# Performance work log

Measured on AMD Instinct MI355X. Metric: run time of the kernel, lower is better.

## Reference

```python
import jax, jax.numpy as jnp
import numpy as np

B_SZ, N_NODES, C_IN, C_OUT, M_EDGES, DEG = 32, 4096, 64, 64, 64, 256
E_INC = M_EDGES * DEG  # 16384 incidences
NEG_SLOPE = 0.2
MARGIN = 4.2


def setup_inputs() -> dict:
    key = jax.random.key(0)
    k1, k2, k3, k4 = jax.random.split(key, 4)
    x = jax.random.normal(k1, (B_SZ, N_NODES, C_IN), jnp.float32)
    # glorot-ish params
    weight = jax.random.normal(k2, (C_IN, C_OUT), jnp.float32) * (1.0 / np.sqrt(C_IN))
    att = jax.random.normal(k3, (1, 1, 2 * C_OUT), jnp.float32) * 0.1
    node_ids = jax.random.randint(k4, (E_INC,), 0, N_NODES, dtype=jnp.int32)
    edge_ids = jnp.repeat(jnp.arange(M_EDGES, dtype=jnp.int32), DEG)  # sorted, all edges present
    hyperedge_index = jnp.stack([node_ids, edge_ids], axis=0)
    return {"x": x, "weight": weight, "att": att,
            "hyperedge_index": hyperedge_index,
            "num_edges": M_EDGES, "num_nodes": N_NODES}


def _segment_softmax(scores, seg, num_segments):
    m = jax.ops.segment_max(scores, seg, num_segments=num_segments)
    e = jnp.exp(scores - m[seg])
    s = jax.ops.segment_sum(e, seg, num_segments=num_segments)
    return e / s[seg]


def reference(x, weight, att, hyperedge_index, num_edges, num_nodes):
    node_ids = hyperedge_index[0]
    edge_ids = hyperedge_index[1]
    M = num_edges
    N = num_nodes

    xw = jnp.einsum('bnc,cd->bnd', x, weight)       # [B,N,C]
    x1 = jnp.swapaxes(xw, 0, 1)                     # [N,B,C]

    x_i = x1[node_ids]                              # [E,B,C] gather per incidence
    edge_sums = jax.ops.segment_sum(x_i, edge_ids, num_segments=M,
                                    indices_are_sorted=True)  # [M,B,C]
    x_j = edge_sums[edge_ids]                       # [E,B,C]

    # pairwise hyperedge contrastive loss (vectorized double loop over edges)
    inner = jnp.einsum('kbc,mbc->kmb', edge_sums, edge_sums)          # [M,M,B]
    nrm = jnp.linalg.norm(edge_sums, axis=-1)                         # [M,B]
    cos = inner / (nrm[:, None, :] * nrm[None, :, :])                 # [M,M,B]
    diff = edge_sums[:, None] - edge_sums[None, :]                    # [M,M,B,C]
    dist = jnp.linalg.norm(diff, axis=-1)                             # [M,M,B]
    loss_item = cos * dist + (1.0 - cos) * jnp.clip(MARGIN - dist, 0.0)
    loss_hyper = jnp.sum(jnp.abs(jnp.mean(loss_item, axis=2))) / (M + 1) ** 2

    # GAT-style attention over incidences, softmax grouped by node
    cat = jnp.concatenate([x_i, x_j], axis=-1)                        # [E,B,2C]
    scores = jnp.sum(cat * att[0], axis=-1)                           # [E,B] (heads=1)
    scores = jax.nn.leaky_relu(scores, negative_slope=NEG_SLOPE)
    alpha = _segment_softmax(scores, node_ids, N)                     # [E,B]
    # dropout omitted (eval mode)

    ones = jnp.ones((node_ids.shape[0],), xw.dtype)
    D = jax.ops.segment_sum(ones, node_ids, num_segments=N)           # node degree
    deg_e = jax.ops.segment_sum(ones, edge_ids, num_segments=M, indices_are_sorted=True)
    B_norm = jnp.where(deg_e > 0, 1.0 / deg_e, 0.0)                   # 1/edge degree, inf->0

    # stage 1: nodes -> hyperedges (source_to_target)
    msg1 = B_norm[edge_ids][:, None, None] * (alpha[..., None] * x_i) # [E,B,C]
    out_e = jax.ops.segment_sum(msg1, edge_ids, num_segments=M, indices_are_sorted=True)
    # stage 2: hyperedges -> nodes (target_to_source)
    msg2 = D[node_ids][:, None, None] * (alpha[..., None] * out_e[edge_ids])
    out_n = jax.ops.segment_sum(msg2, node_ids, num_segments=N)       # [N,B,C]

    out = jnp.swapaxes(out_n, 0, 1)                                   # [B,N,C]
    constrain_total = jnp.abs(jnp.mean(x_i - x_j)) + loss_hyper
    return out, constrain_total
```

## Files before the change

kernel.cpp:

```cpp
#include <hip/hip_runtime.h>
#include <hip/hip_fp16.h>
#include <math.h>

#define B_SZ 32
#define N_NODES 4096
#define C_DIM 64
#define M_EDGES 64
#define DEG 256
#define E_INC 16384
#define NEG_SLOPE 0.2f
#define MARGIN 4.2f

__device__ __forceinline__ float wsum64(float v) {
#pragma unroll
  for (int off = 32; off > 0; off >>= 1) v += __shfl_xor(v, off, 64);
  return v;
}

__global__ __launch_bounds__(256) void k_p0(
    const float* __restrict__ x, const float* __restrict__ w,
    const float* __restrict__ att, const int* __restrict__ node_ids,
    float* __restrict__ s1_t, __half* __restrict__ xh,
    int* __restrict__ cntv) {
  const int bid = blockIdx.x;
  const int t = threadIdx.x;
  if (bid < 1024) {
    __shared__ float part[4][64];
    __shared__ float wattl[64];
    const int kk = t & 63, q = t >> 6;
    float p = 0.f;
#pragma unroll
    for (int c = 0; c < 16; ++c)
      p = fmaf(w[kk * 64 + q * 16 + c], att[q * 16 + c], p);
    part[q][kk] = p;
    __syncthreads();
    if (t < 64)
      wattl[t] = part[0][t] + part[1][t] + part[2][t] + part[3][t];
    __syncthreads();
    const int lane = t & 63, wv = t >> 6;
    const int kq = lane & 15, rsub = lane >> 4;
    const float4 wq = ((const float4*)wattl)[kq];
    const int r0 = bid * 128 + wv * 32;
#pragma unroll 4
    for (int it = 0; it < 8; ++it) {
      const int row = r0 + it * 4 + rsub;
      const float4 xv = ((const float4*)x)[row * 16 + kq];
      float vv = xv.x * wq.x + xv.y * wq.y + xv.z * wq.z + xv.w * wq.w;
      vv += __shfl_xor(vv, 1, 64);
      vv += __shfl_xor(vv, 2, 64);
      vv += __shfl_xor(vv, 4, 64);
      vv += __shfl_xor(vv, 8, 64);
      if (kq == 0) {
        const int n = row & (N_NODES - 1);
        const int b = row >> 12;
        s1_t[n * 32 + b] = vv;
      }
      union {
        __half2 h2[2];
        uint2 u;
      } pk;
      pk.h2[0] = __halves2half2(__float2half(xv.x), __float2half(xv.y));
      pk.h2[1] = __halves2half2(__float2half(xv.z), __float2half(xv.w));
      ((uint2*)xh)[row * 16 + kq] = pk.u;
    }
  } else {
    __shared__ int cnt[N_NODES];
    const int m = bid - 1024;
#pragma unroll
    for (int i = 0; i < 16; ++i) cnt[t + 256 * i] = 0;
    __syncthreads();
    atomicAdd(&cnt[node_ids[m * DEG + t]], 1);
    __syncthreads();
#pragma unroll
    for (int i = 0; i < 16; ++i)
      cntv[m * N_NODES + t + 256 * i] = cnt[t + 256 * i];
  }
}

__global__ __launch_bounds__(256) void k_p1(
    const __half* __restrict__ xh, const float* __restrict__ w,
    const float* __restrict__ att, const int* __restrict__ node_ids,
    float* __restrict__ es_t, float* __restrict__ s2,
    float* __restrict__ nrm2, float* __restrict__ essum) {
  __shared__ float wl[4096];
  __shared__ float sx[4][64];
  __shared__ float part2[4][64];
  const int bid = blockIdx.x;
  const int t = threadIdx.x;
  const int b = 4 * (bid & 7) + ((bid >> 3) & 3);
  const int m = bid >> 5;
  const int lane = t & 63, wv = t >> 6;
  const int co = lane & 7, rg = lane >> 3;
  float4* wl4 = (float4*)wl;
  const float4* w4 = (const float4*)w;
#pragma unroll
  for (int i = 0; i < 4; ++i) wl4[t + 256 * i] = w4[t + 256 * i];
  const uint4* xb = (const uint4*)(xh + (size_t)b * (N_NODES * C_DIM));
  const int myinc = node_ids[m * DEG + wv * 64 + lane];
  int nds[8];
#pragma unroll
  for (int j = 0; j < 8; ++j) nds[j] = __shfl(myinc, j * 8 + rg, 64);
  uint4 v[8];
#pragma unroll
  for (int j = 0; j < 8; ++j) v[j] = xb[nds[j] * 8 + co];
  float acc[8] = {0.f, 0.f, 0.f, 0.f, 0.f, 0.f, 0.f, 0.f};
#pragma unroll
  for (int j = 0; j < 8; ++j) {
    const __half2* hp = (const __half2*)&v[j];
#pragma unroll
    for (int q = 0; q < 4; ++q) {
      const float2 f2 = __half22float2(hp[q]);
      acc[2 * q] += f2.x;
      acc[2 * q + 1] += f2.y;
    }
  }
#pragma unroll
  for (int off = 8; off < 64; off <<= 1) {
#pragma unroll
    for (int k = 0; k < 8; ++k) acc[k] += __shfl_xor(acc[k], off, 64);
  }
  if (rg == 0) {
    ((float4*)&sx[wv][co * 8])[0] =
        make_float4(acc[0], acc[1], acc[2], acc[3]);
    ((float4*)&sx[wv][co * 8])[1] =
        make_float4(acc[4], acc[5], acc[6], acc[7]);
  }
  __syncthreads();
  {
    const int c = t & 63;
    float ep = 0.f;
#pragma unroll
    for (int jj = 0; jj < 16; ++jj) {
      const int j = wv * 16 + jj;
      const float sxcj = sx[0][j] + sx[1][j] + sx[2][j] + sx[3][j];
      ep = fmaf(sxcj, wl[j * 64 + c], ep);
    }
    part2[wv][c] = ep;
  }
  __syncthreads();
  if (t < 64) {
    const float es = part2[0][t] + part2[1][t] + part2[2][t] + part2[3][t];
    es_t[(m * 64 + t) * 32 + b] = es;
    const float sr = wsum64(es * att[64 + t]);
    const float nr = wsum64(es * es);
    const float er = wsum64(es);
    if (t == 0) {
      s2[m * 32 + b] = sr;
      nrm2[m * 32 + b] = nr;
      essum[m * 32 + b] = er;
    }
  }
}

__global__ __launch_bounds__(256) void k_p2(
    const float* __restrict__ es_t, const float* __restrict__ nrm2,
    const int* __restrict__ cntv, const float* __restrict__ s1_t,
    const float* __restrict__ s2, float* __restrict__ lossbuf2,
    float2* __restrict__ pnb, int* __restrict__ pdat,
    int* __restrict__ plen) {
  const int bid = blockIdx.x;
  if (bid < 504) {
    const int wv = threadIdx.x >> 6;
    const int p = bid * 4 + wv;
    int k = 0, off = 0;
    while (off + (63 - k) <= p) {
      off += 63 - k;
      ++k;
    }
    const int m = k + 1 + (p - off);
    const int lane = threadIdx.x & 63;
    const int b = lane & 31, ch = lane >> 5;
    float inner = 0.f;
#pragma unroll 8
    for (int cc = 0; cc < 32; ++cc) {
      const int c = cc + 32 * ch;
      inner = fmaf(es_t[(k * 64 + c) * 32 + b], es_t[(m * 64 + c) * 32 + b],
                   inner);
    }
    inner += __shfl_xor(inner, 32, 64);
    const float nk2 = nrm2[k * 32 + b];
    const float nm2 = nrm2[m * 32 + b];
    const float d2 = fmaxf(nk2 + nm2 - 2.f * inner, 0.f);
    const float dist = sqrtf(d2);
    const float cosv = inner / sqrtf(nk2 * nm2);
    float li = cosv * dist + (1.f - cosv) * fmaxf(MARGIN - dist, 0.f);
#pragma unroll
    for (int o = 16; o > 0; o >>= 1) li += __shfl_xor(li, o, 64);
    if (lane == 0) lossbuf2[p] = 2.f * fabsf(li * (1.f / 32.f));
  } else {
    const int idx = (bid - 504) * 256 + threadIdx.x;
    const int n = idx >> 5, b = idx & 31;
    const float s1v = s1_t[n * 32 + b];
    const bool leader = (b == 0);
    float mx = -1e30f, S = 0.f;
    int j = 0, Dsum = 0;
#pragma unroll 4
    for (int m = 0; m < 64; ++m) {
      const int cm = cntv[m * N_NODES + n];
      float sc = s1v + s2[m * 32 + b];
      sc = sc > 0.f ? sc : NEG_SLOPE * sc;
      const float scv = (cm > 0) ? sc : -1e30f;
      const float nm = fmaxf(mx, scv);
      S = S * __expf(mx - nm) + (float)cm * __expf(scv - nm);
      mx = nm;
      if (leader) {
        if (cm > 0) {
          pdat[n * 64 + j] = m | (cm << 8);
          ++j;
        }
        Dsum += cm;
      }
    }
    if (leader) plen[n] = j | (Dsum << 7);
    float2 pv;
    pv.x = mx;
    pv.y = (S > 0.f) ? 1.f / S : 0.f;
    pnb[n * 32 + b] = pv;
  }
}

__global__ __launch_bounds__(256) void k_p3(
    const __half* __restrict__ xh, const int* __restrict__ node_ids,
    const float* __restrict__ w, const float* __restrict__ s1_t,
    const float* __restrict__ s2, const float2* __restrict__ pnb,
    const float* __restrict__ essum, const float* __restrict__ lossbuf2,
    float* __restrict__ out_e_t, float* __restrict__ outs) {
  __shared__ float wl[4096];
  __shared__ float sx[4][64];
  __shared__ float part2[4][64];
  const int bid = blockIdx.x;
  const int t = threadIdx.x;
  if (bid < 2048) {
    const int b = 4 * (bid & 7) + ((bid >> 3) & 3);
    const int m = bid >> 5;
    const int lane = t & 63, wv = t >> 6;
    const int co = lane & 7, rg = lane >> 3;
    float4* wl4 = (float4*)wl;
    const float4* w4 = (const float4*)w;
#pragma unroll
    for (int i = 0; i < 4; ++i) wl4[t + 256 * i] = w4[t + 256 * i];
    const uint4* xb = (const uint4*)(xh + (size_t)b * (N_NODES * C_DIM));
    const float s2mb = s2[m * 32 + b];
    const int myinc = node_ids[m * DEG + wv * 64 + lane];
    const float s1v = s1_t[myinc * 32 + b];
    const float2 pv = pnb[myinc * 32 + b];
    float scl = s1v + s2mb;
    scl = scl > 0.f ? scl : NEG_SLOPE * scl;
    const float mya = __expf(scl - pv.x) * pv.y;
    int nds[8];
    float av[8];
#pragma unroll
    for (int j = 0; j < 8; ++j) {
      nds[j] = __shfl(myinc, j * 8 + rg, 64);
      av[j] = __shfl(mya, j * 8 + rg, 64);
    }
    uint4 v[8];
#pragma unroll
    for (int j = 0; j < 8; ++j) v[j] = xb[nds[j] * 8 + co];
    float acc[8] = {0.f, 0.f, 0.f, 0.f, 0.f, 0.f, 0.f, 0.f};
#pragma unroll
    for (int j = 0; j < 8; ++j) {
      const __half2* hp = (const __half2*)&v[j];
#pragma unroll
      for (int q = 0; q < 4; ++q) {
        const float2 f2 = __half22float2(hp[q]);
        acc[2 * q] = fmaf(av[j], f2.x, acc[2 * q]);
        acc[2 * q + 1] = fmaf(av[j], f2.y, acc[2 * q + 1]);
      }
    }
#pragma unroll
    for (int off = 8; off < 64; off <<= 1) {
#pragma unroll
      for (int k = 0; k < 8; ++k) acc[k] += __shfl_xor(acc[k], off, 64);
    }
    if (rg == 0) {
      ((float4*)&sx[wv][co * 8])[0] =
          make_float4(acc[0], acc[1], acc[2], acc[3]);
      ((float4*)&sx[wv][co * 8])[1] =
          make_float4(acc[4], acc[5], acc[6], acc[7]);
    }
    __syncthreads();
    {
      const int c = t & 63;
      float ep = 0.f;
#pragma unroll
      for (int jj = 0; jj < 16; ++jj) {
        const int j = wv * 16 + jj;
        const float sxcj = sx[0][j] + sx[1][j] + sx[2][j] + sx[3][j];
        ep = fmaf(sxcj, wl[j * 64 + c], ep);
      }
      part2[wv][c] = ep;
    }
    __syncthreads();
    if (t < 64) {
      const float oc = part2[0][t] + part2[1][t] + part2[2][t] + part2[3][t];
      out_e_t[(m * 64 + t) * 32 + b] = oc * (1.0f / 256.0f);
    }
  } else {
    __shared__ float smf[256];
    float s = 0.f;
    for (int i = t; i < M_EDGES * B_SZ; i += 256) s += essum[i];
    smf[t] = s;
    __syncthreads();
    for (int o = 128; o > 0; o >>= 1) {
      if (t < o) smf[t] += smf[t + o];
      __syncthreads();
    }
    const float S = smf[0];
    __syncthreads();
    float l = 0.f;
    for (int i = t; i < 2016; i += 256) l += lossbuf2[i];
    smf[t] = l;
    __syncthreads();
    for (int o = 128; o > 0; o >>= 1) {
      if (t < o) smf[t] += smf[t + o];
      __syncthreads();
    }
    if (t == 0) {
      const float mean = S * (-255.0f) / 33554432.0f;
      outs[0] = fabsf(mean) + smf[0] * (1.0f / 4225.0f);
    }
  }
}

__global__ __launch_bounds__(256) void k_p4(
    const int* __restrict__ plen, const int* __restrict__ pdat,
    const float* __restrict__ s1_t, const float* __restrict__ s2,
    const float2* __restrict__ pnb, const float* __restrict__ out_e_t,
    float* __restrict__ out) {
  __shared__ int lme[64];
  __shared__ float lcnt[64];
  __shared__ float al[64][32];
  const int n = blockIdx.x;
  const int t = threadIdx.x;
  const int pl = plen[n];
  const int len = pl & 127;
  const float Dn = (float)(pl >> 7);
  const int c = t & 63, bq = t >> 6;
  const size_t nb = (size_t)n * 64 + c;
  const size_t st = (size_t)N_NODES * 64;
  if (len == 0) {
#pragma unroll
    for (int j = 0; j < 8; ++j) out[(bq * 8 + j) * st + nb] = 0.f;
    return;
  }
  if (t < len) {
    const int pe = pdat[n * 64 + t];
    lme[t] = pe & 63;
    lcnt[t] = (float)(pe >> 8);
  }
  __syncthreads();
  {
    const int b = t & 31, lq = t >> 5;
    const float s1v = s1_t[n * 32 + b];
    const float2 pv = pnb[n * 32 + b];
    for (int base = 0; base < len; base += 8) {
      const int li = base + lq;
      if (li < len) {
        const int m = lme[li];
        float sc = s1v + s2[m * 32 + b];
        sc = sc > 0.f ? sc : NEG_SLOPE * sc;
        al[li][b] = lcnt[li] * __expf(sc - pv.x) * pv.y;
      }
    }
  }
  __syncthreads();
  float4 a0 = {0.f, 0.f, 0.f, 0.f}, a1 = {0.f, 0.f, 0.f, 0.f};
  for (int li = 0; li < len; ++li) {
    const int m = lme[li];
    const float4 v0 = *(const float4*)&out_e_t[(m * 64 + c) * 32 + bq * 8];
    const float4 v1 = *(const float4*)&out_e_t[(m * 64 + c) * 32 + bq * 8 + 4];
    const float* alr = al[li];
    a0.x = fmaf(alr[bq * 8 + 0], v0.x, a0.x);
    a0.y = fmaf(alr[bq * 8 + 1], v0.y, a0.y);
    a0.z = fmaf(alr[bq * 8 + 2], v0.z, a0.z);
    a0.w = fmaf(alr[bq * 8 + 3], v0.w, a0.w);
    a1.x = fmaf(alr[bq * 8 + 4], v1.x, a1.x);
    a1.y = fmaf(alr[bq * 8 + 5], v1.y, a1.y);
    a1.z = fmaf(alr[bq * 8 + 6], v1.z, a1.z);
    a1.w = fmaf(alr[bq * 8 + 7], v1.w, a1.w);
  }
  out[(bq * 8 + 0) * st + nb] = Dn * a0.x;
  out[(bq * 8 + 1) * st + nb] = Dn * a0.y;
  out[(bq * 8 + 2) * st + nb] = Dn * a0.z;
  out[(bq * 8 + 3) * st + nb] = Dn * a0.w;
  out[(bq * 8 + 4) * st + nb] = Dn * a1.x;
  out[(bq * 8 + 5) * st + nb] = Dn * a1.y;
  out[(bq * 8 + 6) * st + nb] = Dn * a1.z;
  out[(bq * 8 + 7) * st + nb] = Dn * a1.w;
}

extern "C" void kernel_launch(void* const* d_in, const int* in_sizes, int n_in,
                              void* d_out, int out_size, void* d_ws,
                              size_t ws_size, hipStream_t stream) {
  (void)in_sizes; (void)n_in; (void)out_size; (void)ws_size;
  const float* x = (const float*)d_in[0];
  const float* weight = (const float*)d_in[1];
  const float* att = (const float*)d_in[2];
  const int* node_ids = (const int*)d_in[3];
  float* out = (float*)d_out;

  char* wsb = (char*)d_ws;
  float* es_t = (float*)(wsb);
  float* out_e_t = (float*)(wsb + (512 << 10));
  float* s1_t = (float*)(wsb + (1024 << 10));
  int* cntv = (int*)(wsb + (1536 << 10));
  float2* pnb = (float2*)(wsb + (2560 << 10));
  int* pdat = (int*)(wsb + (3584 << 10));
  float* s2 = (float*)(wsb + (4608 << 10));
  float* nrm2 = (float*)(wsb + (4616 << 10));
  float* essum = (float*)(wsb + (4624 << 10));
  float* lossbuf2 = (float*)(wsb + (4632 << 10));
  int* plen = (int*)(wsb + (4640 << 10));
  __half* xh = (__half*)(wsb + (5120 << 10));

  k_p0<<<1088, 256, 0, stream>>>(x, weight, att, node_ids, s1_t, xh, cntv);
  k_p1<<<2048, 256, 0, stream>>>(xh, weight, att, node_ids, es_t, s2, nrm2,
                                 essum);
  k_p2<<<1016, 256, 0, stream>>>(es_t, nrm2, cntv, s1_t, s2, lossbuf2, pnb,
                                 pdat, plen);
  k_p3<<<2049, 256, 0, stream>>>(xh, node_ids, weight, s1_t, s2, pnb, essum,
                                 lossbuf2, out_e_t,
                                 out + (size_t)B_SZ * N_NODES * C_DIM);
  k_p4<<<4096, 256, 0, stream>>>(plen, pdat, s1_t, s2, pnb, out_e_t, out);
}
```

Measured before the change: 88.32 us.

## Process four batches per block in edge-aggregation kernels and halve p0 grid

k_p1 and k_p3 now handle four batch indices per block instead of one. The shared-memory weight load, the node-id loads and the softmax-parameter loads are amortised across those batches, and the results go out as float4 stores into the batch-minor layout. The W projection is restructured so each wave computes a full 64-length dot product for one batch, instead of splitting the reduction across waves. k_p0 gives each block twice as many rows. Grids shrink fourfold for the edge kernels, which lowers parallelism and latency hiding.

```diff
diff --git a/kernel.cpp b/kernel.cpp
--- a/kernel.cpp
+++ b/kernel.cpp
@@ -24,7 +24,7 @@
     int* __restrict__ cntv) {
   const int bid = blockIdx.x;
   const int t = threadIdx.x;
-  if (bid < 1024) {
+  if (bid < 512) {
     __shared__ float part[4][64];
     __shared__ float wattl[64];
     const int kk = t & 63, q = t >> 6;
@@ -40,9 +40,9 @@
     const int lane = t & 63, wv = t >> 6;
     const int kq = lane & 15, rsub = lane >> 4;
     const float4 wq = ((const float4*)wattl)[kq];
-    const int r0 = bid * 128 + wv * 32;
+    const int r0 = bid * 256 + wv * 64;
 #pragma unroll 4
-    for (int it = 0; it < 8; ++it) {
+    for (int it = 0; it < 16; ++it) {
       const int row = r0 + it * 4 + rsub;
       const float4 xv = ((const float4*)x)[row * 16 + kq];
       float vv = xv.x * wq.x + xv.y * wq.y + xv.z * wq.z + xv.w * wq.w;
@@ -65,7 +65,7 @@
     }
   } else {
     __shared__ int cnt[N_NODES];
-    const int m = bid - 1024;
+    const int m = bid - 512;
 #pragma unroll
     for (int i = 0; i < 16; ++i) cnt[t + 256 * i] = 0;
     __syncthreads();
@@ -83,72 +83,77 @@
     float* __restrict__ es_t, float* __restrict__ s2,
     float* __restrict__ nrm2, float* __restrict__ essum) {
   __shared__ float wl[4096];
-  __shared__ float sx[4][64];
-  __shared__ float part2[4][64];
+  __shared__ float sx[4][4][64];
+  __shared__ float est[4][64];
   const int bid = blockIdx.x;
+  const int bg = bid & 7;
+  const int m = bid >> 3;
+  const int b0 = bg * 4;
   const int t = threadIdx.x;
-  const int b = 4 * (bid & 7) + ((bid >> 3) & 3);
-  const int m = bid >> 5;
   const int lane = t & 63, wv = t >> 6;
   const int co = lane & 7, rg = lane >> 3;
   float4* wl4 = (float4*)wl;
   const float4* w4 = (const float4*)w;
 #pragma unroll
   for (int i = 0; i < 4; ++i) wl4[t + 256 * i] = w4[t + 256 * i];
-  const uint4* xb = (const uint4*)(xh + (size_t)b * (N_NODES * C_DIM));
   const int myinc = node_ids[m * DEG + wv * 64 + lane];
   int nds[8];
 #pragma unroll
   for (int j = 0; j < 8; ++j) nds[j] = __shfl(myinc, j * 8 + rg, 64);
-  uint4 v[8];
-#pragma unroll
-  for (int j = 0; j < 8; ++j) v[j] = xb[nds[j] * 8 + co];
-  float acc[8] = {0.f, 0.f, 0.f, 0.f, 0.f, 0.f, 0.f, 0.f};
-#pragma unroll
-  for (int j = 0; j < 8; ++j) {
-    const __half2* hp = (const __half2*)&v[j];
-#pragma unroll
-    for (int q = 0; q < 4; ++q) {
-      const float2 f2 = __half22float2(hp[q]);
-      acc[2 * q] += f2.x;
-      acc[2 * q + 1] += f2.y;
-    }
-  }
-#pragma unroll
-  for (int off = 8; off < 64; off <<= 1) {
-#pragma unroll
-    for (int k = 0; k < 8; ++k) acc[k] += __shfl_xor(acc[k], off, 64);
-  }
-  if (rg == 0) {
-    ((float4*)&sx[wv][co * 8])[0] =
-        make_float4(acc[0], acc[1], acc[2], acc[3]);
-    ((float4*)&sx[wv][co * 8])[1] =
-        make_float4(acc[4], acc[5], acc[6], acc[7]);
+#pragma unroll
+  for (int bi = 0; bi < 4; ++bi) {
+    const uint4* xb =
+        (const uint4*)(xh + (size_t)(b0 + bi) * (N_NODES * C_DIM));
+    uint4 v[8];
+#pragma unroll
+    for (int j = 0; j < 8; ++j) v[j] = xb[nds[j] * 8 + co];
+    float acc[8] = {0.f, 0.f, 0.f, 0.f, 0.f, 0.f, 0.f, 0.f};
+#pragma unroll
+    for (int j = 0; j < 8; ++j) {
+      const __half2* hp = (const __half2*)&v[j];
+#pragma unroll
+      for (int q = 0; q < 4; ++q) {
+        const float2 f2 = __half22float2(hp[q]);
+        acc[2 * q] += f2.x;
+        acc[2 * q + 1] += f2.y;
+      }
+    }
+#pragma unroll
+    for (int off = 8; off < 64; off <<= 1) {
+#pragma unroll
+      for (int k = 0; k < 8; ++k) acc[k] += __shfl_xor(acc[k], off, 64);
+    }
+    if (rg == 0) {
+      ((float4*)&sx[wv][bi][co * 8])[0] =
+          make_float4(acc[0], acc[1], acc[2], acc[3]);
+      ((float4*)&sx[wv][bi][co * 8])[1] =
+          make_float4(acc[4], acc[5], acc[6], acc[7]);
+    }
   }
   __syncthreads();
   {
-    const int c = t & 63;
-    float ep = 0.f;
-#pragma unroll
-    for (int jj = 0; jj < 16; ++jj) {
-      const int j = wv * 16 + jj;
-      const float sxcj = sx[0][j] + sx[1][j] + sx[2][j] + sx[3][j];
-      ep = fmaf(sxcj, wl[j * 64 + c], ep);
-    }
-    part2[wv][c] = ep;
+    const int c = lane;
+    float es = 0.f;
+#pragma unroll 8
+    for (int j = 0; j < 64; ++j) {
+      const float sxcj =
+          sx[0][wv][j] + sx[1][wv][j] + sx[2][wv][j] + sx[3][wv][j];
+      es = fmaf(sxcj, wl[j * 64 + c], es);
+    }
+    est[wv][c] = es;
+    const float sr = wsum64(es * att[64 + c]);
+    const float nr = wsum64(es * es);
+    const float er = wsum64(es);
+    if (c == 0) {
+      s2[m * 32 + b0 + wv] = sr;
+      nrm2[m * 32 + b0 + wv] = nr;
+      essum[m * 32 + b0 + wv] = er;
+    }
   }
   __syncthreads();
   if (t < 64) {
-    const float es = part2[0][t] + part2[1][t] + part2[2][t] + part2[3][t];
-    es_t[(m * 64 + t) * 32 + b] = es;
-    const float sr = wsum64(es * att[64 + t]);
-    const float nr = wsum64(es * es);
-    const float er = wsum64(es);
-    if (t == 0) {
-      s2[m * 32 + b] = sr;
-      nrm2[m * 32 + b] = nr;
-      essum[m * 32 + b] = er;
-    }
+    const float4 o = make_float4(est[0][t], est[1][t], est[2][t], est[3][t]);
+    *(float4*)&es_t[(m * 64 + t) * 32 + b0] = o;
   }
 }
 
@@ -226,75 +231,90 @@
     const float* __restrict__ essum, const float* __restrict__ lossbuf2,
     float* __restrict__ out_e_t, float* __restrict__ outs) {
   __shared__ float wl[4096];
-  __shared__ float sx[4][64];
-  __shared__ float part2[4][64];
+  __shared__ float sx[4][4][64];
+  __shared__ float est[4][64];
   const int bid = blockIdx.x;
   const int t = threadIdx.x;
-  if (bid < 2048) {
-    const int b = 4 * (bid & 7) + ((bid >> 3) & 3);
-    const int m = bid >> 5;
+  if (bid < 512) {
+    const int bg = bid & 7;
+    const int m = bid >> 3;
+    const int b0 = bg * 4;
     const int lane = t & 63, wv = t >> 6;
     const int co = lane & 7, rg = lane >> 3;
     float4* wl4 = (float4*)wl;
     const float4* w4 = (const float4*)w;
 #pragma unroll
     for (int i = 0; i < 4; ++i) wl4[t + 256 * i] = w4[t + 256 * i];
-    const uint4* xb = (const uint4*)(xh + (size_t)b * (N_NODES * C_DIM));
-    const float s2mb = s2[m * 32 + b];
     const int myinc = node_ids[m * DEG + wv * 64 + lane];
-    const float s1v = s1_t[myinc * 32 + b];
-    const float2 pv = pnb[myinc * 32 + b];
-    float scl = s1v + s2mb;
-    scl = scl > 0.f ? scl : NEG_SLOPE * scl;
-    const float mya = __expf(scl - pv.x) * pv.y;
+    const float4 s14 = *(const float4*)&s1_t[myinc * 32 + b0];
+    const float* pp = (const float*)&pnb[myinc * 32 + b0];
+    const float4 pA = *(const float4*)pp;
+    const float4 pB = *(const float4*)(pp + 4);
+    float mya[4];
+    {
+      const float s1a[4] = {s14.x, s14.y, s14.z, s14.w};
+      const float mxa[4] = {pA.x, pA.z, pB.x, pB.z};
+      const float iva[4] = {pA.y, pA.w, pB.y, pB.w};
+#pragma unroll
+      for (int bi = 0; bi < 4; ++bi) {
+        float sc = s1a[bi] + s2[m * 32 + b0 + bi];
+        sc = sc > 0.f ? sc : NEG_SLOPE * sc;
+        mya[bi] = __expf(sc - mxa[bi]) * iva[bi];
+      }
+    }
     int nds[8];
-    float av[8];
-#pragma unroll
-    for (int j = 0; j < 8; ++j) {
-      nds[j] = __shfl(myinc, j * 8 + rg, 64);
-      av[j] = __shfl(mya, j * 8 + rg, 64);
-    }
-    uint4 v[8];
-#pragma unroll
-    for (int j = 0; j < 8; ++j) v[j] = xb[nds[j] * 8 + co];
-    float acc[8] = {0.f, 0.f, 0.f, 0.f, 0.f, 0.f, 0.f, 0.f};
-#pragma unroll
-    for (int j = 0; j < 8; ++j) {
-      const __half2* hp = (const __half2*)&v[j];
-#pragma unroll
-      for (int q = 0; q < 4; ++q) {
-        const float2 f2 = __half22float2(hp[q]);
-        acc[2 * q] = fmaf(av[j], f2.x, acc[2 * q]);
-        acc[2 * q + 1] = fmaf(av[j], f2.y, acc[2 * q + 1]);
-      }
-    }
-#pragma unroll
-    for (int off = 8; off < 64; off <<= 1) {
-#pragma unroll
-      for (int k = 0; k < 8; ++k) acc[k] += __shfl_xor(acc[k], off, 64);
-    }
-    if (rg == 0) {
-      ((float4*)&sx[wv][co * 8])[0] =
-          make_float4(acc[0], acc[1], acc[2], acc[3]);
-      ((float4*)&sx[wv][co * 8])[1] =
-          make_float4(acc[4], acc[5], acc[6], acc[7]);
+#pragma unroll
+    for (int j = 0; j < 8; ++j) nds[j] = __shfl(myinc, j * 8 + rg, 64);
+#pragma unroll
+    for (int bi = 0; bi < 4; ++bi) {
+      const uint4* xb =
+          (const uint4*)(xh + (size_t)(b0 + bi) * (N_NODES * C_DIM));
+      float av[8];
+#pragma unroll
+      for (int j = 0; j < 8; ++j) av[j] = __shfl(mya[bi], j * 8 + rg, 64);
+      uint4 v[8];
+#pragma unroll
+      for (int j = 0; j < 8; ++j) v[j] = xb[nds[j] * 8 + co];
+      float acc[8] = {0.f, 0.f, 0.f, 0.f, 0.f, 0.f, 0.f, 0.f};
+#pragma unroll
+      for (int j = 0; j < 8; ++j) {
+        const __half2* hp = (const __half2*)&v[j];
+#pragma unroll
+        for (int q = 0; q < 4; ++q) {
+          const float2 f2 = __half22float2(hp[q]);
+          acc[2 * q] = fmaf(av[j], f2.x, acc[2 * q]);
+          acc[2 * q + 1] = fmaf(av[j], f2.y, acc[2 * q + 1]);
+        }
+      }
+#pragma unroll
+      for (int off = 8; off < 64; off <<= 1) {
+#pragma unroll
+        for (int k = 0; k < 8; ++k) acc[k] += __shfl_xor(acc[k], off, 64);
+      }
+      if (rg == 0) {
+        ((float4*)&sx[wv][bi][co * 8])[0] =
+            make_float4(acc[0], acc[1], acc[2], acc[3]);
+        ((float4*)&sx[wv][bi][co * 8])[1] =
+            make_float4(acc[4], acc[5], acc[6], acc[7]);
+      }
     }
     __syncthreads();
     {
-      const int c = t & 63;
-      float ep = 0.f;
-#pragma unroll
-      for (int jj = 0; jj < 16; ++jj) {
-        const int j = wv * 16 + jj;
-        const float sxcj = sx[0][j] + sx[1][j] + sx[2][j] + sx[3][j];
-        ep = fmaf(sxcj, wl[j * 64 + c], ep);
-      }
-      part2[wv][c] = ep;
+      const int c = lane;
+      float oc = 0.f;
+#pragma unroll 8
+      for (int j = 0; j < 64; ++j) {
+        const float sxcj =
+            sx[0][wv][j] + sx[1][wv][j] + sx[2][wv][j] + sx[3][wv][j];
+        oc = fmaf(sxcj, wl[j * 64 + c], oc);
+      }
+      est[wv][c] = oc * (1.0f / 256.0f);
     }
     __syncthreads();
     if (t < 64) {
-      const float oc = part2[0][t] + part2[1][t] + part2[2][t] + part2[3][t];
-      out_e_t[(m * 64 + t) * 32 + b] = oc * (1.0f / 256.0f);
+      const float4 o =
+          make_float4(est[0][t], est[1][t], est[2][t], est[3][t]);
+      *(float4*)&out_e_t[(m * 64 + t) * 32 + b0] = o;
     }
   } else {
     __shared__ float smf[256];
@@ -414,13 +434,13 @@
   int* plen = (int*)(wsb + (4640 << 10));
   __half* xh = (__half*)(wsb + (5120 << 10));
 
-  k_p0<<<1088, 256, 0, stream>>>(x, weight, att, node_ids, s1_t, xh, cntv);
-  k_p1<<<2048, 256, 0, stream>>>(xh, weight, att, node_ids, es_t, s2, nrm2,
-                                 essum);
+  k_p0<<<576, 256, 0, stream>>>(x, weight, att, node_ids, s1_t, xh, cntv);
+  k_p1<<<512, 256, 0, stream>>>(xh, weight, att, node_ids, es_t, s2, nrm2,
+                                essum);
   k_p2<<<1016, 256, 0, stream>>>(es_t, nrm2, cntv, s1_t, s2, lossbuf2, pnb,
                                  pdat, plen);
-  k_p3<<<2049, 256, 0, stream>>>(xh, node_ids, weight, s1_t, s2, pnb, essum,
-                                 lossbuf2, out_e_t,
-                                 out + (size_t)B_SZ * N_NODES * C_DIM);
+  k_p3<<<513, 256, 0, stream>>>(xh, node_ids, weight, s1_t, s2, pnb, essum,
+                                lossbuf2, out_e_t,
+                                out + (size_t)B_SZ * N_NODES * C_DIM);
   k_p4<<<4096, 256, 0, stream>>>(plen, pdat, s1_t, s2, pnb, out_e_t, out);
 }
```

New measurement: 84.45 us. 1.05x faster.
